# Kernel optimization log

Measured on AMD Instinct MI355X. Metric: run time of the kernel, lower is better.

The kernel has to match this reference:

```python
import jax, jax.numpy as jnp
import numpy as np

B, L, D = 4, 2048, 256
EXPAND, D_STATE, D_CONV = 2, 16, 4
D_INNER = EXPAND * D
DT_RANK = (D + 15) // 16  # ceil(d_model/16) = 16
N_HEADS = 4
H_MLP = int(D * 4.0)
EPS = 1e-5


def _ln(x, w, b):
    mu = x.mean(-1, keepdims=True)
    var = ((x - mu) ** 2).mean(-1, keepdims=True)
    return (x - mu) / jnp.sqrt(var + EPS) * w + b


def _silu(x):
    return x * jax.nn.sigmoid(x)


def _mamba(x, Win, convw, convb, Wx, Wdt, bdt, Alog, Dp, Wout):
    # x: (B, L, D) -> (B, L, D). Standard Mamba mixer (selective scan).
    b, l, d = x.shape
    xz = x @ Win.T                      # (b, l, 2*d_inner)
    xi, z = jnp.split(xz, 2, axis=-1)
    # depthwise causal conv1d, kernel D_CONV
    xc = jnp.swapaxes(xi, 1, 2)         # (b, d_inner, l)
    xc = jax.lax.conv_general_dilated(
        xc, convw, (1,), [(D_CONV - 1, 0)],
        feature_group_count=D_INNER, dimension_numbers=('NCW', 'OIW', 'NCW'))
    xi = _silu(jnp.swapaxes(xc + convb[None, :, None], 1, 2))  # (b, l, d_inner)
    dbl = xi @ Wx.T                     # (b, l, dt_rank + 2*d_state)
    dt = jax.nn.softplus(dbl[..., :DT_RANK] @ Wdt.T + bdt)     # (b, l, d_inner)
    Bm = dbl[..., DT_RANK:DT_RANK + D_STATE]                    # (b, l, n)
    Cm = dbl[..., DT_RANK + D_STATE:]                            # (b, l, n)
    A = -jnp.exp(Alog)                  # (d_inner, n)

    def step(h, ins):
        dt_t, B_t, C_t, u_t = ins       # (b,d_inner),(b,n),(b,n),(b,d_inner)
        h = h * jnp.exp(dt_t[..., None] * A) + dt_t[..., None] * B_t[:, None, :] * u_t[..., None]
        return h, jnp.einsum('bdn,bn->bd', h, C_t)

    xs = tuple(jnp.swapaxes(t, 0, 1) for t in (dt, Bm, Cm, xi))  # time-major
    h0 = jnp.zeros((b, D_INNER, D_STATE), x.dtype)
    _, ys = jax.lax.scan(step, h0, xs)  # ys: (l, b, d_inner)
    y = jnp.swapaxes(ys, 0, 1) + xi * Dp
    return (y * _silu(z)) @ Wout.T


def _attn(x, Wqkv, bqkv, Wo, bo):
    b, l, d = x.shape
    hd = d // N_HEADS
    qkv = x @ Wqkv.T + bqkv
    q, k, v = jnp.split(qkv, 3, axis=-1)
    sh = lambda t: t.reshape(b, l, N_HEADS, hd).transpose(0, 2, 1, 3)
    q, k, v = sh(q), sh(k), sh(v)
    a = jax.nn.softmax(jnp.einsum('bhqd,bhkd->bhqk', q, k) / np.float32(np.sqrt(hd)), axis=-1)
    o = jnp.einsum('bhqk,bhkd->bhqd', a, v).transpose(0, 2, 1, 3).reshape(b, l, d)
    return o @ Wo.T + bo


def setup_inputs() -> dict:
    key = jax.random.key(0)
    ks = iter(jax.random.split(key, 40))
    rn = lambda shape, s=0.02: jax.random.normal(next(ks), shape, jnp.float32) * s
    inp = {'x': jax.random.normal(next(ks), (B, L, D), jnp.float32)}
    for p in ('mf', 'mb'):
        inp[p + '_Win'] = rn((2 * D_INNER, D))
        inp[p + '_convw'] = rn((D_INNER, 1, D_CONV), 0.1)
        inp[p + '_convb'] = jnp.zeros((D_INNER,), jnp.float32)
        inp[p + '_Wx'] = rn((DT_RANK + 2 * D_STATE, D_INNER))
        inp[p + '_Wdt'] = rn((D_INNER, DT_RANK), 0.1)
        inp[p + '_bdt'] = rn((D_INNER,), 0.5)
        inp[p + '_Alog'] = jnp.log(jnp.broadcast_to(jnp.arange(1, D_STATE + 1, dtype=jnp.float32), (D_INNER, D_STATE)))
        inp[p + '_D'] = jnp.ones((D_INNER,), jnp.float32)
        inp[p + '_Wout'] = rn((D, D_INNER))
    for n in ('n1', 'n2', 'n3'):
        inp[n + 'w'] = jnp.ones((D,), jnp.float32)
        inp[n + 'b'] = jnp.zeros((D,), jnp.float32)
    inp['Wqkv'] = rn((3 * D, D))
    inp['bqkv'] = jnp.zeros((3 * D,), jnp.float32)
    inp['Wo'] = rn((D, D))
    inp['bo'] = jnp.zeros((D,), jnp.float32)
    inp['fc1w'] = rn((H_MLP, D))
    inp['fc1b'] = jnp.zeros((H_MLP,), jnp.float32)
    inp['fc2w'] = rn((D, H_MLP))
    inp['fc2b'] = jnp.zeros((D,), jnp.float32)
    return inp


def reference(x, n1w, n1b, n2w, n2b, n3w, n3b,
              mf_Win, mf_convw, mf_convb, mf_Wx, mf_Wdt, mf_bdt, mf_Alog, mf_D, mf_Wout,
              mb_Win, mb_convw, mb_convb, mb_Wx, mb_Wdt, mb_bdt, mb_Alog, mb_D, mb_Wout,
              Wqkv, bqkv, Wo, bo, fc1w, fc1b, fc2w, fc2b):
    # Mamba branch (bidirectional): DropPath is identity at eval
    h = _ln(x, n1w, n1b)
    fwd = _mamba(h, mf_Win, mf_convw, mf_convb, mf_Wx, mf_Wdt, mf_bdt, mf_Alog, mf_D, mf_Wout)
    bwd = jnp.flip(_mamba(jnp.flip(h, 1), mb_Win, mb_convw, mb_convb, mb_Wx, mb_Wdt, mb_bdt, mb_Alog, mb_D, mb_Wout), 1)
    x = x + fwd + bwd
    # Attention branch (full attention since window=None)
    x = x + _attn(_ln(x, n2w, n2b), Wqkv, bqkv, Wo, bo)
    # MLP branch (exact GELU like torch default)
    h = _ln(x, n3w, n3b)
    x = x + (jax.nn.gelu(h @ fc1w.T + fc1b, approximate=False) @ fc2w.T + fc2b)
    return x
```

## Files before the change

### kernel.cpp

```cpp
#include <hip/hip_runtime.h>
#include <hip/hip_bf16.h>
#include <math.h>

#define LL 2048
#define DD 256
#define MTOT 8192
#define DINNER 512
#define CT 32
#define NC 64

typedef __attribute__((ext_vector_type(8))) short short8;
typedef __attribute__((ext_vector_type(4))) float f32x4;

__device__ __forceinline__ float us2f(unsigned short u){
  return __uint_as_float(((unsigned)u) << 16);
}
__device__ __forceinline__ unsigned short f2us(float f){
  __hip_bfloat16 h = __float2bfloat16(f);
  return *(unsigned short*)&h;
}
__device__ __forceinline__ float frcp(float x){
  return __builtin_amdgcn_rcpf(x);
}

__global__ void probe_kernel(const unsigned* __restrict__ alog, int* __restrict__ flag){
  if (threadIdx.x == 0 && blockIdx.x == 0) *flag = (alog[0] != 0u) ? 1 : 0;
}

struct Srcs { const void* p[32]; unsigned off[33]; unsigned foff[32]; };

__global__ __launch_bounds__(256) void cvt_all_kernel(Srcs s, float* __restrict__ dst,
                                                      unsigned short* __restrict__ db,
                                                      const int* __restrict__ flag,
                                                      unsigned total){
  unsigned i = blockIdx.x * 256u + threadIdx.x;
  if (i >= total) return;
  int k = 31;
  while (s.off[k] > i) --k;
  unsigned j = i - s.off[k];
  float v;
  if (*flag) v = us2f(((const unsigned short*)s.p[k])[j]);
  else       v = ((const float*)s.p[k])[j];
  if ((k == 24 && j < 65536u) || (k == 25 && j < 256u)) v *= 0.125f;
  db[i] = f2us(v);
  if (s.foff[k] != 0xFFFFFFFFu) dst[s.foff[k] + j] = v;
}

__global__ __launch_bounds__(256) void cvt_x_kernel(const void* __restrict__ src,
                                                    float* __restrict__ dst,
                                                    const int* __restrict__ flag, unsigned n){
  unsigned i = blockIdx.x * 256u + threadIdx.x;
  if (i >= n) return;
  if (*flag) dst[i] = us2f(((const unsigned short*)src)[i]);
  else       dst[i] = ((const float*)src)[i];
}

__global__ __launch_bounds__(256) void wdbl_prep_kernel(
    const float* __restrict__ Wx, int dsWx, unsigned short* __restrict__ Wd)
{
  const unsigned g = blockIdx.x * 256u + threadIdx.x;
  const int dir = g >> 15;
  const unsigned idx = g & 32767u;
  const int n = idx >> 9, k = idx & 511;
  float v = (n < 48) ? (Wx + (size_t)dir * dsWx)[(size_t)n * 512 + k] : 0.f;
  Wd[g] = f2us(v);
}

__global__ __launch_bounds__(256) void final_out_kernel(
    const float* __restrict__ xf, void* __restrict__ out,
    const int* __restrict__ flag, unsigned n)
{
  unsigned i = blockIdx.x * 256u + threadIdx.x;
  if (i >= n) return;
  float v = xf[i];
  if (*flag) ((unsigned short*)out)[i] = f2us(v);
  else       ((float*)out)[i] = v;
}

enum { G_BF16=0, G_GELU=1, G_RESID=2, G_STF=3 };
__global__ __launch_bounds__(256) void gemm_mfma_kernel(
    const unsigned short* __restrict__ A, int lda, int agap,
    const unsigned short* __restrict__ W, const unsigned short* __restrict__ W2,
    int Kw, int nsplit, int ksplit, int msplit,
    const float* __restrict__ bias,
    unsigned short* __restrict__ Cb, float* __restrict__ resid,
    int N, int K, int kslices, int mode)
{
  __shared__ unsigned short sA[64][40];
  __shared__ unsigned short sW[64][40];
  const int tid = threadIdx.x;
  const int w = tid >> 6, lane = tid & 63, quad = lane >> 4, l16 = lane & 15;
  const int m0 = blockIdx.y << 6, n0 = blockIdx.x << 6;
  const int ks = blockIdx.z;
  const int kper = K / kslices;
  const int srow = tid >> 2, skc = (tid & 3) << 3;
  int wr = n0 + srow;
  const unsigned short* Wbase = W;
  if (msplit && m0 >= msplit) Wbase = W2;
  if (nsplit && wr >= nsplit){ Wbase = W2; wr -= nsplit; }
  f32x4 acc[4] = {};
  for (int k0 = ks * kper; k0 < ks * kper + kper; k0 += 32){
    int ac = k0 + skc;
    if (agap && ac >= 512) ac += 512;
    short8 av = *(const short8*)(A + (size_t)(m0 + srow) * lda + ac);
    int kk = k0 + skc;
    const unsigned short* Wp = Wbase;
    if (ksplit && kk >= ksplit){ Wp = W2; kk -= ksplit; }
    short8 wv = *(const short8*)(Wp + (size_t)wr * Kw + kk);
    __syncthreads();
    *(short8*)&sA[srow][skc] = av;
    *(short8*)&sW[srow][skc] = wv;
    __syncthreads();
    short8 af = *(const short8*)&sA[w * 16 + l16][quad << 3];
    #pragma unroll
    for (int ns = 0; ns < 4; ++ns){
      short8 wf = *(const short8*)&sW[ns * 16 + l16][quad << 3];
      acc[ns] = __builtin_amdgcn_mfma_f32_16x16x32_bf16(af, wf, acc[ns], 0, 0, 0);
    }
  }
  #pragma unroll
  for (int ns = 0; ns < 4; ++ns){
    const int n = n0 + ns * 16 + l16;
    const float bv = (bias && ks == 0) ? bias[n] : 0.f;
    #pragma unroll
    for (int r = 0; r < 4; ++r){
      const int m = m0 + w * 16 + quad * 4 + r;
      const size_t off = (size_t)m * N + n;
      float v = acc[ns][r] + bv;
      if (mode == G_BF16) Cb[off] = f2us(v);
      else if (mode == G_GELU) Cb[off] = f2us(0.5f * v * (1.f + erff(v * 0.70710678118f)));
      else if (mode == G_RESID) resid[off] += v;
      else resid[off] = v;
    }
  }
}

__global__ __launch_bounds__(256) void gemm128_kernel(
    const unsigned short* __restrict__ A, int lda,
    const unsigned short* __restrict__ W, const unsigned short* __restrict__ W2,
    int Kw, int nsplit, const float* __restrict__ bias,
    unsigned short* __restrict__ Cb, int N, int K, int mode)
{
  __shared__ unsigned short sA[128][40];
  __shared__ unsigned short sW[128][40];
  const int tid = threadIdx.x;
  const int w = tid >> 6, lane = tid & 63, quad = lane >> 4, l16 = lane & 15;
  const int wm = (w >> 1) << 6, wn = (w & 1) << 6;
  const int m0 = blockIdx.y << 7, n0 = blockIdx.x << 7;
  const int srow = tid >> 2, skc = (tid & 3) << 3;
  const unsigned short* wrp0;
  const unsigned short* wrp1;
  {
    int r0 = n0 + srow, r1 = n0 + srow + 64;
    const unsigned short* b0 = W;
    const unsigned short* b1 = W;
    if (nsplit){
      if (r0 >= nsplit){ b0 = W2; r0 -= nsplit; }
      if (r1 >= nsplit){ b1 = W2; r1 -= nsplit; }
    }
    wrp0 = b0 + (size_t)r0 * Kw;
    wrp1 = b1 + (size_t)r1 * Kw;
  }
  const unsigned short* arp0 = A + (size_t)(m0 + srow) * lda;
  const unsigned short* arp1 = A + (size_t)(m0 + srow + 64) * lda;
  f32x4 acc[4][4] = {};
  for (int k0 = 0; k0 < K; k0 += 32){
    short8 av0 = *(const short8*)(arp0 + k0 + skc);
    short8 av1 = *(const short8*)(arp1 + k0 + skc);
    short8 wv0 = *(const short8*)(wrp0 + k0 + skc);
    short8 wv1 = *(const short8*)(wrp1 + k0 + skc);
    __syncthreads();
    *(short8*)&sA[srow][skc] = av0;
    *(short8*)&sA[srow + 64][skc] = av1;
    *(short8*)&sW[srow][skc] = wv0;
    *(short8*)&sW[srow + 64][skc] = wv1;
    __syncthreads();
    short8 af[4], wf[4];
    #pragma unroll
    for (int i = 0; i < 4; ++i){
      af[i] = *(const short8*)&sA[wm + i * 16 + l16][quad << 3];
      wf[i] = *(const short8*)&sW[wn + i * 16 + l16][quad << 3];
    }
    #pragma unroll
    for (int mi = 0; mi < 4; ++mi)
      #pragma unroll
      for (int ni = 0; ni < 4; ++ni)
        acc[mi][ni] = __builtin_amdgcn_mfma_f32_16x16x32_bf16(af[mi], wf[ni], acc[mi][ni], 0, 0, 0);
  }
  #pragma unroll
  for (int ni = 0; ni < 4; ++ni){
    const int n = n0 + wn + ni * 16 + l16;
    const float bv = bias ? bias[n] : 0.f;
    #pragma unroll
    for (int mi = 0; mi < 4; ++mi){
      #pragma unroll
      for (int r = 0; r < 4; ++r){
        const int m = m0 + wm + mi * 16 + quad * 4 + r;
        float v = acc[mi][ni][r] + bv;
        if (mode == G_GELU) v = 0.5f * v * (1.f + erff(v * 0.70710678118f));
        Cb[(size_t)m * N + n] = f2us(v);
      }
    }
  }
}

__global__ __launch_bounds__(256) void ln_kernel(
    const float* __restrict__ xin,
    const float* __restrict__ w, const float* __restrict__ b,
    unsigned short* __restrict__ hout)
{
  const int row = blockIdx.x, tid = threadIdx.x;
  const size_t off = (size_t)row * DD + tid;
  float v = xin[off];
  float s = v, s2 = v * v;
  #pragma unroll
  for (int o = 32; o; o >>= 1){ s += __shfl_xor(s, o); s2 += __shfl_xor(s2, o); }
  __shared__ float ls[4], ls2[4];
  if ((tid & 63) == 0){ ls[tid >> 6] = s; ls2[tid >> 6] = s2; }
  __syncthreads();
  s  = ls[0] + ls[1] + ls[2] + ls[3];
  s2 = ls2[0] + ls2[1] + ls2[2] + ls2[3];
  const float mu  = s * (1.f / DD);
  const float var = s2 * (1.f / DD) - mu * mu;
  const float inv = rsqrtf(var + 1e-5f);
  hout[off] = f2us((v - mu) * inv * w[tid] + b[tid]);
}

__global__ __launch_bounds__(256) void conv_silu_kernel(
    const unsigned short* __restrict__ xzc, const float* __restrict__ convw0, int dsCw,
    const float* __restrict__ convb0, int dsCb, unsigned short* __restrict__ xi)
{
  const unsigned g = blockIdx.x * 256u + threadIdx.x;
  const int c4 = (g & 127) << 2;
  const int t = (g >> 7) & 2047;
  const int b = (g >> 18) & 3;
  const int dir = g >> 20;
  const float* cw = convw0 + (size_t)dir * dsCw;
  float4 acc = *(const float4*)(convb0 + (size_t)dir * dsCb + c4);
  float wv[4][4];
  #pragma unroll
  for (int j = 0; j < 4; ++j) *(float4*)wv[j] = *(const float4*)(cw + (c4 + j) * 4);
  #pragma unroll
  for (int k = 0; k < 4; ++k){
    const int tt = dir ? (t + (3 - k)) : (t - 3 + k);
    if ((unsigned)tt < 2048u){
      ushort4 x = *(const ushort4*)(xzc + ((size_t)(b * 2048 + tt)) * 2048 + dir * 1024 + c4);
      acc.x = fmaf(wv[0][k], us2f(x.x), acc.x);
      acc.y = fmaf(wv[1][k], us2f(x.y), acc.y);
      acc.z = fmaf(wv[2][k], us2f(x.z), acc.z);
      acc.w = fmaf(wv[3][k], us2f(x.w), acc.w);
    }
  }
  ushort4 o;
  o.x = f2us(acc.x * frcp(1.f + __expf(-acc.x)));
  o.y = f2us(acc.y * frcp(1.f + __expf(-acc.y)));
  o.z = f2us(acc.z * frcp(1.f + __expf(-acc.z)));
  o.w = f2us(acc.w * frcp(1.f + __expf(-acc.w)));
  *(ushort4*)(xi + (size_t)dir * 4194304 + ((size_t)(b * 2048 + t)) * 512 + c4) = o;
}

__global__ __launch_bounds__(256) void scan_part1_kernel(
    const unsigned short* __restrict__ xib, int dsXi,
    const float* __restrict__ dblc,
    const float* __restrict__ Alog, int dsAl,
    const float* __restrict__ Wdt0, int dsWdt,
    const float* __restrict__ bdt0, int dsBdt,
    float* __restrict__ dtsum, int dsDts,
    float* __restrict__ hend, int dsHend)
{
  const int bx = blockIdx.x;
  const int dg = bx & 1, c = (bx >> 1) & (NC - 1), b = (bx >> 7) & 3, dir = bx >> 9;
  const int tid = threadIdx.x;
  const int d = dg * 256 + tid;
  const unsigned short* xi_ = xib + (size_t)dir * dsXi;
  const float* Al_ = Alog + (size_t)dir * dsAl;
  __shared__ float sDB[CT][32];
  __shared__ unsigned short sXI[CT][256];
  {
    const int s = tid >> 3, c4 = (tid & 7) << 2;
    const int t = dir ? (LL - 1 - (c * CT + s)) : (c * CT + s);
    *(float4*)&sDB[s][c4] =
      *(const float4*)(dblc + ((size_t)(dir * 8192 + b * LL + t)) * 64 + c4);
  }
  #pragma unroll
  for (int p = 0; p < 4; ++p){
    const int s = p * 8 + (tid >> 5);
    const int dc = (tid & 31) << 3;
    const int t = dir ? (LL - 1 - (c * CT + s)) : (c * CT + s);
    *(short8*)&sXI[s][dc] =
      *(const short8*)(xi_ + ((size_t)(b * LL + t)) * 512 + dg * 256 + dc);
  }
  float wdt[16];
  {
    const float* wr = Wdt0 + (size_t)dir * dsWdt + (size_t)d * 16;
    #pragma unroll
    for (int q = 0; q < 4; ++q) *(float4*)&wdt[q * 4] = *(const float4*)(wr + q * 4);
  }
  const float bdtd = (bdt0 + (size_t)dir * dsBdt)[d];
  float A[16];
  #pragma unroll
  for (int n = 0; n < 16; ++n) A[n] = -__expf(Al_[d * 16 + n]);
  const float A1 = A[0];
  bool fast = true;
  #pragma unroll
  for (int n = 0; n < 16; ++n)
    fast = fast && (fabsf(A[n] - A1 * (n + 1)) <= 1e-4f * fabsf(A1 * (n + 1)) + 1e-30f);
  __syncthreads();
  float h[16];
  #pragma unroll
  for (int n = 0; n < 16; ++n) h[n] = 0.f;
  float dts = 0.f;
  #pragma unroll 1
  for (int s = 0; s < CT; ++s){
    const float uv = us2f(sXI[s][tid]);
    f32x4 dv[4], Bv[4];
    #pragma unroll
    for (int q = 0; q < 4; ++q) dv[q] = *(const f32x4*)&sDB[s][q * 4];
    #pragma unroll
    for (int q = 0; q < 4; ++q) Bv[q] = *(const f32x4*)&sDB[s][16 + q * 4];
    float p0 = 0.f, p1 = 0.f, p2 = 0.f, p3 = 0.f;
    #pragma unroll
    for (int j = 0; j < 4; ++j){
      p0 = fmaf(dv[0][j], wdt[j],      p0);
      p1 = fmaf(dv[1][j], wdt[4 + j],  p1);
      p2 = fmaf(dv[2][j], wdt[8 + j],  p2);
      p3 = fmaf(dv[3][j], wdt[12 + j], p3);
    }
    const float dtpre = bdtd + ((p0 + p1) + (p2 + p3));
    const float dtv = (dtpre > 20.f) ? dtpre : __logf(1.f + __expf(dtpre));
    const float dtu = dtv * uv;
    dts += dtv;
    if (fast){
      const float e1 = __expf(dtv * A1);
      const float e2 = e1 * e1;
      float eo = e1, ev = e2;
      #pragma unroll
      for (int m = 0; m < 8; ++m){
        h[2 * m]     = fmaf(h[2 * m],     eo, dtu * Bv[(2 * m) >> 2][(2 * m) & 3]);
        h[2 * m + 1] = fmaf(h[2 * m + 1], ev, dtu * Bv[(2 * m + 1) >> 2][(2 * m + 1) & 3]);
        eo *= e2; ev *= e2;
      }
    } else {
      #pragma unroll
      for (int n = 0; n < 16; ++n){
        const float e = __expf(dtv * A[n]);
        h[n] = fmaf(h[n], e, dtu * Bv[n >> 2][n & 3]);
      }
    }
  }
  const size_t base = (size_t)dir * dsHend + ((size_t)((b * NC + c) * 512 + d)) * 16;
  #pragma unroll
  for (int q = 0; q < 4; ++q) *(float4*)&hend[base + q * 4] = *(const float4*)&h[q * 4];
  dtsum[(size_t)dir * dsDts + (size_t)(b * NC + c) * 512 + d] = dts;
}

__global__ __launch_bounds__(256) void scan_combine_kernel(
    const float* __restrict__ dtsum, int dsDts,
    float* __restrict__ hend, int dsHend,
    const float* __restrict__ Alog, int dsAl)
{
  const unsigned g = blockIdx.x * 256u + threadIdx.x;
  const int dir = g >> 15;
  const unsigned gg = g & 32767u;
  const int b = gg >> 13, d = (gg >> 4) & 511, n = gg & 15;
  const float A = -__expf((Alog + (size_t)dir * dsAl)[d * 16 + n]);
  const float* dts_ = dtsum + (size_t)dir * dsDts;
  float* he_ = hend + (size_t)dir * dsHend;
  float h = 0.f;
  for (int c = 0; c < NC; ++c){
    const size_t sb = ((size_t)((b * NC + c) * 512 + d)) * 16 + n;
    const float e = __expf(dts_[(size_t)(b * NC + c) * 512 + d] * A);
    const float he = he_[sb];
    he_[sb] = h;
    h = h * e + he;
  }
}

__global__ __launch_bounds__(256) void scan_part2_kernel(
    const unsigned short* __restrict__ xib, int dsXi,
    const float* __restrict__ dblc,
    const unsigned short* __restrict__ zin,
    unsigned short* __restrict__ yout,
    const float* __restrict__ Alog, int dsAl,
    const float* __restrict__ Wdt0, int dsWdt,
    const float* __restrict__ bdt0, int dsBdt,
    const float* __restrict__ Dp, int dsD,
    const float* __restrict__ hin, int dsHend)
{
  const int bx = blockIdx.x;
  const int dg = bx & 1, c = (bx >> 1) & (NC - 1), b = (bx >> 7) & 3, dir = bx >> 9;
  const int tid = threadIdx.x;
  const int d = dg * 256 + tid;
  const unsigned short* xi_ = xib + (size_t)dir * dsXi;
  const unsigned short* z_ = zin + dir * 1024;
  unsigned short* y_ = yout + dir * 1024;
  const float* Al_ = Alog + (size_t)dir * dsAl;
  __shared__ float sDB[CT][48];
  __shared__ unsigned short sXI[CT][256];
  __shared__ unsigned short sZ[CT][256];
  for (int i4 = tid; i4 < 384; i4 += 256){
    const int s = i4 / 12, cc = (i4 - s * 12) << 2;
    const int t = dir ? (LL - 1 - (c * CT + s)) : (c * CT + s);
    *(float4*)&sDB[s][cc] =
      *(const float4*)(dblc + ((size_t)(dir * 8192 + b * LL + t)) * 64 + cc);
  }
  #pragma unroll
  for (int p = 0; p < 4; ++p){
    const int s = p * 8 + (tid >> 5);
    const int dc = (tid & 31) << 3;
    const int t = dir ? (LL - 1 - (c * CT + s)) : (c * CT + s);
    const size_t row = (size_t)(b * LL + t);
    *(short8*)&sXI[s][dc] = *(const short8*)(xi_ + row * 512 + dg * 256 + dc);
    *(short8*)&sZ[s][dc]  = *(const short8*)(z_ + row * 2048 + dg * 256 + dc);
  }
  float wdt[16];
  {
    const float* wr = Wdt0 + (size_t)dir * dsWdt + (size_t)d * 16;
    #pragma unroll
    for (int q = 0; q < 4; ++q) *(float4*)&wdt[q * 4] = *(const float4*)(wr + q * 4);
  }
  const float bdtd = (bdt0 + (size_t)dir * dsBdt)[d];
  float A[16];
  #pragma unroll
  for (int n = 0; n < 16; ++n) A[n] = -__expf(Al_[d * 16 + n]);
  const float A1 = A[0];
  bool fast = true;
  #pragma unroll
  for (int n = 0; n < 16; ++n)
    fast = fast && (fabsf(A[n] - A1 * (n + 1)) <= 1e-4f * fabsf(A1 * (n + 1)) + 1e-30f);
  const float Dv = (Dp + (size_t)dir * dsD)[d];
  __syncthreads();
  float h[16];
  const size_t base = (size_t)dir * dsHend + ((size_t)((b * NC + c) * 512 + d)) * 16;
  #pragma unroll
  for (int q = 0; q < 4; ++q) *(float4*)&h[q * 4] = *(const float4*)&hin[base + q * 4];
  #pragma unroll 1
  for (int s = 0; s < CT; ++s){
    const int t = dir ? (LL - 1 - (c * CT + s)) : (c * CT + s);
    const size_t row = (size_t)(b * LL + t);
    const float uv = us2f(sXI[s][tid]);
    const float z  = us2f(sZ[s][tid]);
    f32x4 dv[4];
    #pragma unroll
    for (int q = 0; q < 4; ++q) dv[q] = *(const f32x4*)&sDB[s][q * 4];
    float p0 = 0.f, p1 = 0.f, p2 = 0.f, p3 = 0.f;
    #pragma unroll
    for (int j = 0; j < 4; ++j){
      p0 = fmaf(dv[0][j], wdt[j],      p0);
      p1 = fmaf(dv[1][j], wdt[4 + j],  p1);
      p2 = fmaf(dv[2][j], wdt[8 + j],  p2);
      p3 = fmaf(dv[3][j], wdt[12 + j], p3);
    }
    const float dtpre = bdtd + ((p0 + p1) + (p2 + p3));
    const float dtv = (dtpre > 20.f) ? dtpre : __logf(1.f + __expf(dtpre));
    const float dtu = dtv * uv;
    f32x4 Bv[4], Cv[4];
    #pragma unroll
    for (int q = 0; q < 4; ++q) Bv[q] = *(const f32x4*)&sDB[s][16 + q * 4];
    #pragma unroll
    for (int q = 0; q < 4; ++q) Cv[q] = *(const f32x4*)&sDB[s][32 + q * 4];
    float pA = uv * Dv, pB = 0.f;
    if (fast){
      const float e1 = __expf(dtv * A1);
      const float e2 = e1 * e1;
      float eo = e1, ev = e2;
      #pragma unroll
      for (int m = 0; m < 8; ++m){
        const int n0 = 2 * m, n1 = 2 * m + 1;
        h[n0] = fmaf(h[n0], eo, dtu * Bv[n0 >> 2][n0 & 3]);
        pA = fmaf(h[n0], Cv[n0 >> 2][n0 & 3], pA);
        h[n1] = fmaf(h[n1], ev, dtu * Bv[n1 >> 2][n1 & 3]);
        pB = fmaf(h[n1], Cv[n1 >> 2][n1 & 3], pB);
        eo *= e2; ev *= e2;
      }
    } else {
      #pragma unroll
      for (int n = 0; n < 16; ++n){
        const float e = __expf(dtv * A[n]);
        h[n] = fmaf(h[n], e, dtu * Bv[n >> 2][n & 3]);
        pA = fmaf(h[n], Cv[n >> 2][n & 3], pA);
      }
    }
    const float p = pA + pB;
    const float sig = frcp(1.f + __expf(-z));
    y_[row * 2048 + d] = f2us(p * z * sig);
  }
}

__global__ __launch_bounds__(256) void v_prep_kernel(
    const unsigned short* __restrict__ qkvb, unsigned short* __restrict__ Vt)
{
  const int kt = blockIdx.x;
  const int bh = blockIdx.y;
  const int b = bh >> 2, h = bh & 3;
  __shared__ unsigned short tile[64][72];
  #pragma unroll
  for (int rr = 0; rr < 4; ++rr){
    const int idx = (rr * 256 + threadIdx.x) * 4;
    const int key = idx >> 6, d = idx & 63;
    ushort4 v = *(const ushort4*)(qkvb + ((size_t)(b * 2048 + kt * 64 + key)) * 768 + 512 + h * 64 + d);
    *(ushort4*)&tile[key][d] = v;
  }
  __syncthreads();
  #pragma unroll
  for (int rr = 0; rr < 8; ++rr){
    const int o2 = rr * 256 + threadIdx.x;
    const int d = o2 >> 5, k2 = (o2 & 31) << 1;
    ushort2 u;
    u.x = tile[k2][d];
    u.y = tile[k2 + 1][d];
    *(ushort2*)(Vt + (size_t)bh * 131072 + (size_t)d * 2048 + kt * 64 + k2) = u;
  }
}

__global__ __launch_bounds__(256) void attn_mfma_kernel(
    const unsigned short* __restrict__ qkvb, const unsigned short* __restrict__ Vt,
    float* __restrict__ op0, float* __restrict__ op1, float* __restrict__ lpart)
{
  __shared__ unsigned short sK[64][72];
  __shared__ unsigned short sV[64][72];
  __shared__ unsigned short sP[4][32][68];
  const int tid = threadIdx.x;
  const int w = tid >> 6, lane = tid & 63, quad = lane >> 4, l16 = lane & 15;
  const int bh = blockIdx.y;
  const int b = bh >> 2, h = bh & 3;
  const int q0 = blockIdx.x * 128;
  const int split = blockIdx.z;

  short8 qf[2][2];
  #pragma unroll
  for (int qs = 0; qs < 2; ++qs){
    const unsigned short* qp = qkvb + ((size_t)(b * 2048 + q0 + w * 32 + qs * 16 + l16)) * 768 + h * 64 + quad * 8;
    qf[qs][0] = *(const short8*)qp;
    qf[qs][1] = *(const short8*)(qp + 32);
  }

  f32x4 o[2][4] = {};
  float lsum[2][4] = {};

  const int kt0 = split * 512;
  for (int kt = kt0; kt < kt0 + 512; kt += 64){
    __syncthreads();
    #pragma unroll
    for (int r = 0; r < 2; ++r){
      const int idx = (r * 256 + tid) * 8;
      const int row = idx >> 6, c = idx & 63;
      *(short8*)&sK[row][c] = *(const short8*)(qkvb + ((size_t)(b * 2048 + kt + row)) * 768 + 256 + h * 64 + c);
      *(short8*)&sV[row][c] = *(const short8*)(Vt + (size_t)bh * 131072 + (size_t)row * 2048 + kt + c);
    }
    __syncthreads();

    #pragma unroll
    for (int qs = 0; qs < 2; ++qs){
      float p[4][4];
      #pragma unroll
      for (int sub = 0; sub < 4; ++sub){
        short8 bk0 = *(const short8*)&sK[sub * 16 + l16][quad * 8];
        short8 bk1 = *(const short8*)&sK[sub * 16 + l16][32 + quad * 8];
        f32x4 acc = {0,0,0,0};
        acc = __builtin_amdgcn_mfma_f32_16x16x32_bf16(qf[qs][0], bk0, acc, 0, 0, 0);
        acc = __builtin_amdgcn_mfma_f32_16x16x32_bf16(qf[qs][1], bk1, acc, 0, 0, 0);
        #pragma unroll
        for (int r = 0; r < 4; ++r) p[sub][r] = __expf(acc[r]);
      }
      #pragma unroll
      for (int r = 0; r < 4; ++r)
        lsum[qs][r] += p[0][r] + p[1][r] + p[2][r] + p[3][r];
      #pragma unroll
      for (int sub = 0; sub < 4; ++sub)
        #pragma unroll
        for (int r = 0; r < 4; ++r)
          sP[w][qs * 16 + quad * 4 + r][sub * 16 + l16] = f2us(p[sub][r]);
    }
    __builtin_amdgcn_s_waitcnt(0);
    #pragma unroll
    for (int qs = 0; qs < 2; ++qs){
      short8 pa0 = *(const short8*)&sP[w][qs * 16 + l16][quad * 8];
      short8 pa1 = *(const short8*)&sP[w][qs * 16 + l16][32 + quad * 8];
      #pragma unroll
      for (int nsub = 0; nsub < 4; ++nsub){
        short8 bv0 = *(const short8*)&sV[nsub * 16 + l16][quad * 8];
        short8 bv1 = *(const short8*)&sV[nsub * 16 + l16][32 + quad * 8];
        o[qs][nsub] = __builtin_amdgcn_mfma_f32_16x16x32_bf16(pa0, bv0, o[qs][nsub], 0, 0, 0);
        o[qs][nsub] = __builtin_amdgcn_mfma_f32_16x16x32_bf16(pa1, bv1, o[qs][nsub], 0, 0, 0);
      }
    }
  }

  float* op = (split < 2 ? op0 : op1) + (size_t)(split & 1) * 2097152;
  #pragma unroll
  for (int qs = 0; qs < 2; ++qs){
    #pragma unroll
    for (int r = 0; r < 4; ++r){
      float l = lsum[qs][r];
      l += __shfl_xor(l, 1); l += __shfl_xor(l, 2);
      l += __shfl_xor(l, 4); l += __shfl_xor(l, 8);
      const int q = q0 + w * 32 + qs * 16 + quad * 4 + r;
      #pragma unroll
      for (int nsub = 0; nsub < 4; ++nsub)
        op[((size_t)bh * 2048 + q) * 64 + nsub * 16 + l16] = o[qs][nsub][r];
      if (l16 == 0) lpart[(split * 16 + bh) * 2048 + q] = l;
    }
  }
}

__global__ __launch_bounds__(256) void attn_merge_kernel(
    const float* __restrict__ op0, const float* __restrict__ op1,
    const float* __restrict__ lpart, unsigned short* __restrict__ outp)
{
  const unsigned g = blockIdx.x * 256u + threadIdx.x;
  const int d4 = (g & 15) << 2;
  const int q = (g >> 4) & 2047;
  const int bh = g >> 15;
  float4 s = make_float4(0.f, 0.f, 0.f, 0.f);
  float l = 0.f;
  #pragma unroll
  for (int sp = 0; sp < 4; ++sp){
    const float* op = (sp < 2 ? op0 : op1) + (size_t)(sp & 1) * 2097152;
    float4 o = *(const float4*)(op + ((size_t)bh * 2048 + q) * 64 + d4);
    s.x += o.x; s.y += o.y; s.z += o.z; s.w += o.w;
    l += lpart[(sp * 16 + bh) * 2048 + q];
  }
  const float invl = 1.f / l;
  const int b = bh >> 2, h = bh & 3;
  ushort4 u;
  u.x = f2us(s.x * invl);
  u.y = f2us(s.y * invl);
  u.z = f2us(s.z * invl);
  u.w = f2us(s.w * invl);
  *(ushort4*)(outp + ((size_t)(b * 2048 + q)) * 256 + h * 64 + d4) = u;
}

extern "C" void kernel_launch(void* const* d_in, const int* in_sizes, int n_in,
                              void* d_out, int out_size, void* d_ws, size_t ws_size,
                              hipStream_t stream)
{
  static const bool needf[33] = {
    false, false,true,true,true,true,true,true,true,false,
    false,true,true,true,true,true,true,true,false,
    true,true,true,true,true,true,
    false,true,false,true,false,true,false,true };

  int* flag  = (int*)d_ws;
  float* wts = (float*)d_ws + 16;

  Srcs srcs;
  unsigned acc = 0, facc = 0;
  unsigned foff_h[33];
  for (int i = 1; i <= 32; ++i){
    srcs.p[i - 1] = d_in[i];
    srcs.off[i - 1] = acc;
    acc += (unsigned)in_sizes[i];
    if (needf[i]){ srcs.foff[i - 1] = facc; foff_h[i] = facc; facc += (unsigned)in_sizes[i]; }
    else { srcs.foff[i - 1] = 0xFFFFFFFFu; foff_h[i] = 0xFFFFFFFFu; }
  }
  srcs.off[32] = acc;
  const unsigned wtotal = acc;
  const unsigned ftot = (facc + 3u) & ~3u;

  unsigned short* wb16 = (unsigned short*)(wts + ftot);
  float* xf    = wts + ftot + (wtotal + 1) / 2;
  float* xzc_f = xf + 2097152;
  float* xi_f  = xzc_f + 8388608;
  float* dblc  = xi_f + 4194304;
  float* hb_f  = dblc + 1048576;
  float* hend  = hb_f + 1048576;
  float* dtsum = hend + 4194304;
  float* wd_f  = dtsum + 262144;

  unsigned short* xzc  = (unsigned short*)xzc_f;
  unsigned short* xi16 = (unsigned short*)xi_f;
  unsigned short* hb16 = (unsigned short*)hb_f;
  unsigned short* wdbl = (unsigned short*)wd_f;
  unsigned short* qkvb = xzc;
  unsigned short* Vt   = (unsigned short*)hend;
  float* op0   = xzc_f + 4194304;
  float* op1   = xi_f;
  float* lpart = dtsum;
  unsigned short* fc1o = xzc;

  auto wp  = [&](int i){ return wts + foff_h[i]; };
  auto wp16= [&](int i){ return wb16 + srcs.off[i - 1]; };

  hipLaunchKernelGGL(probe_kernel, dim3(1), dim3(64), 0, stream,
      (const unsigned*)d_in[7], flag);
  hipLaunchKernelGGL(cvt_all_kernel, dim3((wtotal + 255) / 256), dim3(256), 0, stream,
      srcs, wts, wb16, flag, wtotal);
  hipLaunchKernelGGL(cvt_x_kernel, dim3(MTOT * DD / 256), dim3(256), 0, stream,
      d_in[0], xf, flag, (unsigned)(MTOT * DD));

  const int dsCw = (int)(foff_h[11] - foff_h[2]);
  const int dsAl = (int)(foff_h[16] - foff_h[7]);
  const int dsD  = (int)(foff_h[17] - foff_h[8]);
  const int dsWx = (int)(foff_h[13] - foff_h[4]);
  const int dsWdt= (int)(foff_h[14] - foff_h[5]);
  const int dsBdt= (int)(foff_h[15] - foff_h[6]);
  const int dsCb2= (int)(foff_h[12] - foff_h[3]);

  hipLaunchKernelGGL(wdbl_prep_kernel, dim3(256), dim3(256), 0, stream,
      wp(4), dsWx, wdbl);

  auto gemm16 = [&](const unsigned short* Ab, int lda, int agap, int M,
                    const unsigned short* W, const unsigned short* W2,
                    int Kw, int nsplit, int ksplit, int msplit, const float* bias,
                    unsigned short* Cb, float* resid,
                    int N, int K, int ksl, int mode){
    hipLaunchKernelGGL(gemm_mfma_kernel, dim3(N / 64, M / 64, ksl), dim3(256), 0, stream,
        Ab, lda, agap, W, W2, Kw, nsplit, ksplit, msplit, bias, Cb, resid, N, K, ksl, mode);
  };
  auto gemm128 = [&](const unsigned short* Ab, int lda, int M,
                     const unsigned short* W, const unsigned short* W2,
                     int Kw, int nsplit, const float* bias,
                     unsigned short* Cb, int N, int K, int mode){
    hipLaunchKernelGGL(gemm128_kernel, dim3(N / 128, M / 128), dim3(256), 0, stream,
        Ab, lda, W, W2, Kw, nsplit, bias, Cb, N, K, mode);
  };

  hipLaunchKernelGGL(ln_kernel, dim3(MTOT), dim3(256), 0, stream,
      xf, wp(19), wp(20), hb16);

  gemm128(hb16, 256, MTOT, wp16(1), wp16(10), 256, 1024, nullptr,
          xzc, 2048, 256, G_BF16);
  hipLaunchKernelGGL(conv_silu_kernel, dim3(8192), dim3(256), 0, stream,
      xzc, wp(2), dsCw, wp(3), dsCb2, xi16);
  gemm16(xi16, 512, 0, 2 * MTOT, wdbl, wdbl + 32768, 512, 0, 0, MTOT, nullptr,
         nullptr, dblc, 64, 512, 1, G_STF);
  hipLaunchKernelGGL(scan_part1_kernel, dim3(1024), dim3(256), 0, stream,
      xi16, 4194304, dblc, wp(7), dsAl, wp(5), dsWdt, wp(6), dsBdt,
      dtsum, 131072, hend, 2097152);
  hipLaunchKernelGGL(scan_combine_kernel, dim3(256), dim3(256), 0, stream,
      dtsum, 131072, hend, 2097152, wp(7), dsAl);
  hipLaunchKernelGGL(scan_part2_kernel, dim3(1024), dim3(256), 0, stream,
      xi16, 4194304, dblc, xzc + 512, xzc, wp(7), dsAl, wp(5), dsWdt, wp(6), dsBdt,
      wp(8), dsD, hend, 2097152);
  gemm16(xzc, 2048, 1, MTOT, wp16(9), wp16(18), 512, 0, 512, 0, nullptr,
         nullptr, xf, 256, 1024, 1, G_RESID);

  hipLaunchKernelGGL(ln_kernel, dim3(MTOT), dim3(256), 0, stream,
      xf, wp(21), wp(22), hb16);
  gemm128(hb16, 256, MTOT, wp16(25), nullptr, 256, 0, wp(26),
          qkvb, 768, 256, G_BF16);
  hipLaunchKernelGGL(v_prep_kernel, dim3(32, 16), dim3(256), 0, stream,
      qkvb, Vt);
  hipLaunchKernelGGL(attn_mfma_kernel, dim3(16, 16, 4), dim3(256), 0, stream,
      qkvb, Vt, op0, op1, lpart);
  hipLaunchKernelGGL(attn_merge_kernel, dim3(2048), dim3(256), 0, stream,
      op0, op1, lpart, hb16);
  gemm16(hb16, 256, 0, MTOT, wp16(27), nullptr, 256, 0, 0, 0, wp(28),
         nullptr, xf, 256, 256, 1, G_RESID);

  hipLaunchKernelGGL(ln_kernel, dim3(MTOT), dim3(256), 0, stream,
      xf, wp(23), wp(24), hb16);
  gemm128(hb16, 256, MTOT, wp16(29), nullptr, 256, 0, wp(30),
          fc1o, 1024, 256, G_GELU);
  gemm16(fc1o, 1024, 0, MTOT, wp16(31), nullptr, 1024, 0, 0, 0, nullptr,
         nullptr, xf, 256, 1024, 1, G_RESID);
  hipLaunchKernelGGL(final_out_kernel, dim3(MTOT * DD / 256), dim3(256), 0, stream,
      xf, d_out, flag, (unsigned)(MTOT * DD));
}
```

Baseline: 439.9 us.

## Fuse input conversion into first LN, output into last GEMM, parallelize scan combine

The input cast kernel is folded into a new first LayerNorm kernel that also writes the fp32 residual copy. The final output conversion is fused into the fc2 GEMM epilogue through a new G_OUT mode that adds the residual and writes bf16 or fp32 directly. The serial per-thread chunk-combine loop in the scan is replaced by a wavefront-wide Hillis-Steele associative scan over the 64 chunks, one wave per (dir,b,d,n), with a much larger grid. This removes two elementwise passes over the activations and the serial combine latency, at the cost of more threads and shuffles in the combine.

Result: slower. 473.6 us (+7.7%).

```diff
diff --git a/kernel.cpp b/kernel.cpp
--- a/kernel.cpp
+++ b/kernel.cpp
@@ -46,15 +46,6 @@
   if (s.foff[k] != 0xFFFFFFFFu) dst[s.foff[k] + j] = v;
 }
 
-__global__ __launch_bounds__(256) void cvt_x_kernel(const void* __restrict__ src,
-                                                    float* __restrict__ dst,
-                                                    const int* __restrict__ flag, unsigned n){
-  unsigned i = blockIdx.x * 256u + threadIdx.x;
-  if (i >= n) return;
-  if (*flag) dst[i] = us2f(((const unsigned short*)src)[i]);
-  else       dst[i] = ((const float*)src)[i];
-}
-
 __global__ __launch_bounds__(256) void wdbl_prep_kernel(
     const float* __restrict__ Wx, int dsWx, unsigned short* __restrict__ Wd)
 {
@@ -66,25 +57,15 @@
   Wd[g] = f2us(v);
 }
 
-__global__ __launch_bounds__(256) void final_out_kernel(
-    const float* __restrict__ xf, void* __restrict__ out,
-    const int* __restrict__ flag, unsigned n)
-{
-  unsigned i = blockIdx.x * 256u + threadIdx.x;
-  if (i >= n) return;
-  float v = xf[i];
-  if (*flag) ((unsigned short*)out)[i] = f2us(v);
-  else       ((float*)out)[i] = v;
-}
-
-enum { G_BF16=0, G_GELU=1, G_RESID=2, G_STF=3 };
+enum { G_BF16=0, G_GELU=1, G_RESID=2, G_STF=3, G_OUT=4 };
 __global__ __launch_bounds__(256) void gemm_mfma_kernel(
     const unsigned short* __restrict__ A, int lda, int agap,
     const unsigned short* __restrict__ W, const unsigned short* __restrict__ W2,
     int Kw, int nsplit, int ksplit, int msplit,
     const float* __restrict__ bias,
     unsigned short* __restrict__ Cb, float* __restrict__ resid,
-    int N, int K, int kslices, int mode)
+    int N, int K, int kslices, int mode,
+    const int* __restrict__ flag, void* __restrict__ outp)
 {
   __shared__ unsigned short sA[64][40];
   __shared__ unsigned short sW[64][40];
@@ -94,6 +75,7 @@
   const int ks = blockIdx.z;
   const int kper = K / kslices;
   const int srow = tid >> 2, skc = (tid & 3) << 3;
+  const int fl = flag ? *flag : 0;
   int wr = n0 + srow;
   const unsigned short* Wbase = W;
   if (msplit && m0 >= msplit) Wbase = W2;
@@ -130,7 +112,12 @@
       if (mode == G_BF16) Cb[off] = f2us(v);
       else if (mode == G_GELU) Cb[off] = f2us(0.5f * v * (1.f + erff(v * 0.70710678118f)));
       else if (mode == G_RESID) resid[off] += v;
-      else resid[off] = v;
+      else if (mode == G_STF) resid[off] = v;
+      else {
+        const float t = v + resid[off];
+        if (fl) ((unsigned short*)outp)[off] = f2us(t);
+        else    ((float*)outp)[off] = t;
+      }
     }
   }
 }
@@ -226,6 +213,32 @@
   hout[off] = f2us((v - mu) * inv * w[tid] + b[tid]);
 }
 
+__global__ __launch_bounds__(256) void ln_first_kernel(
+    const void* __restrict__ src, const int* __restrict__ flag,
+    float* __restrict__ xf,
+    const float* __restrict__ w, const float* __restrict__ b,
+    unsigned short* __restrict__ hout)
+{
+  const int row = blockIdx.x, tid = threadIdx.x;
+  const size_t off = (size_t)row * DD + tid;
+  float v;
+  if (*flag) v = us2f(((const unsigned short*)src)[off]);
+  else       v = ((const float*)src)[off];
+  xf[off] = v;
+  float s = v, s2 = v * v;
+  #pragma unroll
+  for (int o = 32; o; o >>= 1){ s += __shfl_xor(s, o); s2 += __shfl_xor(s2, o); }
+  __shared__ float ls[4], ls2[4];
+  if ((tid & 63) == 0){ ls[tid >> 6] = s; ls2[tid >> 6] = s2; }
+  __syncthreads();
+  s  = ls[0] + ls[1] + ls[2] + ls[3];
+  s2 = ls2[0] + ls2[1] + ls2[2] + ls2[3];
+  const float mu  = s * (1.f / DD);
+  const float var = s2 * (1.f / DD) - mu * mu;
+  const float inv = rsqrtf(var + 1e-5f);
+  hout[off] = f2us((v - mu) * inv * w[tid] + b[tid]);
+}
+
 __global__ __launch_bounds__(256) void conv_silu_kernel(
     const unsigned short* __restrict__ xzc, const float* __restrict__ convw0, int dsCw,
     const float* __restrict__ convb0, int dsCb, unsigned short* __restrict__ xi)
@@ -359,21 +372,26 @@
     float* __restrict__ hend, int dsHend,
     const float* __restrict__ Alog, int dsAl)
 {
-  const unsigned g = blockIdx.x * 256u + threadIdx.x;
-  const int dir = g >> 15;
-  const unsigned gg = g & 32767u;
-  const int b = gg >> 13, d = (gg >> 4) & 511, n = gg & 15;
+  const int tid = threadIdx.x;
+  const int lane = tid & 63;
+  const unsigned gw = blockIdx.x * 4u + (tid >> 6);
+  const int n = gw & 15, d = (gw >> 4) & 511, b = (gw >> 13) & 3, dir = gw >> 15;
   const float A = -__expf((Alog + (size_t)dir * dsAl)[d * 16 + n]);
   const float* dts_ = dtsum + (size_t)dir * dsDts;
   float* he_ = hend + (size_t)dir * dsHend;
-  float h = 0.f;
-  for (int c = 0; c < NC; ++c){
-    const size_t sb = ((size_t)((b * NC + c) * 512 + d)) * 16 + n;
-    const float e = __expf(dts_[(size_t)(b * NC + c) * 512 + d] * A);
-    const float he = he_[sb];
-    he_[sb] = h;
-    h = h * e + he;
-  }
+  const int c = lane;
+  const size_t sb = ((size_t)((b * NC + c) * 512 + d)) * 16 + n;
+  float E = __expf(dts_[(size_t)(b * NC + c) * 512 + d] * A);
+  float H = he_[sb];
+  #pragma unroll
+  for (int off = 1; off < 64; off <<= 1){
+    const float Eu = __shfl_up(E, off);
+    const float Hu = __shfl_up(H, off);
+    if (lane >= off){ H = fmaf(Hu, E, H); E = Eu * E; }
+  }
+  float hin = __shfl_up(H, 1);
+  if (lane == 0) hin = 0.f;
+  he_[sb] = hin;
 }
 
 __global__ __launch_bounds__(256) void scan_part2_kernel(
@@ -686,8 +704,6 @@
       (const unsigned*)d_in[7], flag);
   hipLaunchKernelGGL(cvt_all_kernel, dim3((wtotal + 255) / 256), dim3(256), 0, stream,
       srcs, wts, wb16, flag, wtotal);
-  hipLaunchKernelGGL(cvt_x_kernel, dim3(MTOT * DD / 256), dim3(256), 0, stream,
-      d_in[0], xf, flag, (unsigned)(MTOT * DD));
 
   const int dsCw = (int)(foff_h[11] - foff_h[2]);
   const int dsAl = (int)(foff_h[16] - foff_h[7]);
@@ -704,9 +720,10 @@
                     const unsigned short* W, const unsigned short* W2,
                     int Kw, int nsplit, int ksplit, int msplit, const float* bias,
                     unsigned short* Cb, float* resid,
-                    int N, int K, int ksl, int mode){
+                    int N, int K, int ksl, int mode, void* outp = nullptr){
     hipLaunchKernelGGL(gemm_mfma_kernel, dim3(N / 64, M / 64, ksl), dim3(256), 0, stream,
-        Ab, lda, agap, W, W2, Kw, nsplit, ksplit, msplit, bias, Cb, resid, N, K, ksl, mode);
+        Ab, lda, agap, W, W2, Kw, nsplit, ksplit, msplit, bias, Cb, resid, N, K, ksl, mode,
+        (const int*)flag, outp);
   };
   auto gemm128 = [&](const unsigned short* Ab, int lda, int M,
                      const unsigned short* W, const unsigned short* W2,
@@ -716,8 +733,8 @@
         Ab, lda, W, W2, Kw, nsplit, bias, Cb, N, K, mode);
   };
 
-  hipLaunchKernelGGL(ln_kernel, dim3(MTOT), dim3(256), 0, stream,
-      xf, wp(19), wp(20), hb16);
+  hipLaunchKernelGGL(ln_first_kernel, dim3(MTOT), dim3(256), 0, stream,
+      d_in[0], flag, xf, wp(19), wp(20), hb16);
 
   gemm128(hb16, 256, MTOT, wp16(1), wp16(10), 256, 1024, nullptr,
           xzc, 2048, 256, G_BF16);
@@ -728,7 +745,7 @@
   hipLaunchKernelGGL(scan_part1_kernel, dim3(1024), dim3(256), 0, stream,
       xi16, 4194304, dblc, wp(7), dsAl, wp(5), dsWdt, wp(6), dsBdt,
       dtsum, 131072, hend, 2097152);
-  hipLaunchKernelGGL(scan_combine_kernel, dim3(256), dim3(256), 0, stream,
+  hipLaunchKernelGGL(scan_combine_kernel, dim3(16384), dim3(256), 0, stream,
       dtsum, 131072, hend, 2097152, wp(7), dsAl);
   hipLaunchKernelGGL(scan_part2_kernel, dim3(1024), dim3(256), 0, stream,
       xi16, 4194304, dblc, xzc + 512, xzc, wp(7), dsAl, wp(5), dsWdt, wp(6), dsBdt,
@@ -754,7 +771,5 @@
   gemm128(hb16, 256, MTOT, wp16(29), nullptr, 256, 0, wp(30),
           fc1o, 1024, 256, G_GELU);
   gemm16(fc1o, 1024, 0, MTOT, wp16(31), nullptr, 1024, 0, 0, 0, nullptr,
-         nullptr, xf, 256, 1024, 1, G_RESID);
-  hipLaunchKernelGGL(final_out_kernel, dim3(MTOT * DD / 256), dim3(256), 0, stream,
-      xf, d_out, flag, (unsigned)(MTOT * DD));
-}
+         nullptr, xf, 256, 1024, 1, G_OUT, d_out);
+}
```
